# Optimization experiments

Hardware: AMD Instinct MI355X
Metric: run time of the kernel (lower is better)

Reference implementation:

```python
import jax, jax.numpy as jnp
from jax import lax
import numpy as np


def setup_inputs() -> dict:
    key = jax.random.key(0)
    k1, k2 = jax.random.split(key)
    x = jax.random.normal(k1, (16, 512, 512, 3), dtype=jnp.float32)
    # raw filter; module draws N(mean=10, scale=1) then normalizes to sum 1
    filt = jax.random.normal(k2, (9, 9, 1, 1), dtype=jnp.float32)
    return {"x": x, "filt": filt}


def _conv_same(a, f):
    # NHWC input, HWIO filter, SAME padding, stride 1
    return lax.conv_general_dilated(
        a, f, window_strides=(1, 1), padding="SAME",
        dimension_numbers=("NHWC", "HWIO", "NHWC"))


def reference(x, filt):
    # Keras: random_normal_variable(mean=10, scale=1) -> shift raw N(0,1) by 10
    f = filt + 10.0
    f = f / jnp.sum(f)                      # normalize BEFORE channel repeat
    f = jnp.tile(f, (1, 1, 3, 1))           # (9,9,3,1): sums over 3 input channels
    local_mean = _conv_same(x, f)           # (B,H,W,1), broadcasts over channels
    v = x - local_mean                      # (B,H,W,3)
    sigma = jnp.sqrt(_conv_same(v * v, f))  # (B,H,W,1)
    mean = jnp.mean(sigma, axis=(1, 2), keepdims=True)  # (B,1,1,1)
    return v / jnp.maximum(mean, sigma)
```

## Files before the change

### kernel.cpp

```cpp
#include <hip/hip_runtime.h>

#define BATCH 16
#define HH 512
#define WW 512
#define NPIX (BATCH * HH * WW)

#define TW 32
#define TH 8
#define ROWS 4
#define OTH (TH*ROWS)
#define RAD 4
#define LW (TW + 2 * RAD)
#define LH (OTH + 2 * RAD)

__global__ void norm_filter_kernel(const float* __restrict__ filt,
                                   float* __restrict__ f) {
    __shared__ float sh[128];
    int tid = threadIdx.x;
    float v = (tid < 81) ? (filt[tid] + 10.0f) : 0.0f;
    sh[tid] = v;
    __syncthreads();
    for (int o = 64; o > 0; o >>= 1) {
        if (tid < o) sh[tid] += sh[tid + o];
        __syncthreads();
    }
    float sum = sh[0];
    if (tid < 81) f[tid] = v / sum;
}

__global__ __launch_bounds__(256) void conv_mean_kernel(
        const float* __restrict__ x, const float* __restrict__ f,
        float* __restrict__ m, float* __restrict__ t) {
    __shared__ float tile[LH][LW];
    __shared__ float fs[81];

    const int tx = threadIdx.x, ty = threadIdx.y;
    const int tid = ty * TW + tx;
    const int b = blockIdx.z;
    const int h0 = blockIdx.y * OTH;
    const int w0 = blockIdx.x * TW;
    const float* xb = x + (size_t)b * HH * WW * 3;

    for (int i = tid; i < LH * LW; i += 256) {
        int r = i / LW, c = i - r * LW;
        int gh = h0 - RAD + r, gw = w0 - RAD + c;
        float v = 0.0f;
        if (gh >= 0 && gh < HH && gw >= 0 && gw < WW) {
            const float* xp = xb + ((size_t)gh * WW + gw) * 3;
            v = xp[0] + xp[1] + xp[2];
        }
        tile[r][c] = v;
    }
    if (tid < 81) fs[tid] = f[tid];
    __syncthreads();

    const int r0 = ty * ROWS;
    float acc[ROWS] = {0.f, 0.f, 0.f, 0.f};
#pragma unroll
    for (int tr = 0; tr < ROWS + 8; tr++) {
        float v[9];
#pragma unroll
        for (int j = 0; j < 9; j++) v[j] = tile[r0 + tr][tx + j];
#pragma unroll
        for (int o = 0; o < ROWS; o++) {
            const int dh = tr - o;
            if (dh >= 0 && dh < 9) {
#pragma unroll
                for (int j = 0; j < 9; j++) acc[o] += v[j] * fs[dh * 9 + j];
            }
        }
    }

#pragma unroll
    for (int o = 0; o < ROWS; o++) {
        const int h = h0 + r0 + o, w = w0 + tx;
        const size_t idx = ((size_t)b * HH + h) * WW + w;
        m[idx] = acc[o];
        const float* xp = xb + ((size_t)h * WW + w) * 3;
        float d0 = xp[0] - acc[o];
        float d1 = xp[1] - acc[o];
        float d2 = xp[2] - acc[o];
        t[idx] = d0 * d0 + d1 * d1 + d2 * d2;
    }
}

__global__ __launch_bounds__(256) void conv_sigma_kernel(
        const float* __restrict__ t, const float* __restrict__ f,
        float* __restrict__ sig, float* __restrict__ partial) {
    __shared__ float tile[LH][LW];
    __shared__ float fs[81];
    __shared__ float wsum[4];

    const int tx = threadIdx.x, ty = threadIdx.y;
    const int tid = ty * TW + tx;
    const int b = blockIdx.z;
    const int h0 = blockIdx.y * OTH;
    const int w0 = blockIdx.x * TW;
    const float* tb = t + (size_t)b * HH * WW;

    for (int i = tid; i < LH * LW; i += 256) {
        int r = i / LW, c = i - r * LW;
        int gh = h0 - RAD + r, gw = w0 - RAD + c;
        float v = 0.0f;
        if (gh >= 0 && gh < HH && gw >= 0 && gw < WW) {
            v = tb[(size_t)gh * WW + gw];
        }
        tile[r][c] = v;
    }
    if (tid < 81) fs[tid] = f[tid];
    __syncthreads();

    const int r0 = ty * ROWS;
    float acc[ROWS] = {0.f, 0.f, 0.f, 0.f};
#pragma unroll
    for (int tr = 0; tr < ROWS + 8; tr++) {
        float v[9];
#pragma unroll
        for (int j = 0; j < 9; j++) v[j] = tile[r0 + tr][tx + j];
#pragma unroll
        for (int o = 0; o < ROWS; o++) {
            const int dh = tr - o;
            if (dh >= 0 && dh < 9) {
#pragma unroll
                for (int j = 0; j < 9; j++) acc[o] += v[j] * fs[dh * 9 + j];
            }
        }
    }

    float psum = 0.0f;
#pragma unroll
    for (int o = 0; o < ROWS; o++) {
        float sg = sqrtf(fmaxf(acc[o], 0.0f));
        const int h = h0 + r0 + o, w = w0 + tx;
        sig[((size_t)b * HH + h) * WW + w] = sg;
        psum += sg;
    }

#pragma unroll
    for (int o = 32; o > 0; o >>= 1) psum += __shfl_down(psum, o);
    if ((tid & 63) == 0) wsum[tid >> 6] = psum;
    __syncthreads();
    if (tid == 0)
        partial[b * 256 + blockIdx.y * 16 + blockIdx.x] =
            wsum[0] + wsum[1] + wsum[2] + wsum[3];
}

__global__ __launch_bounds__(256) void reduce_bsum_kernel(
        const float* __restrict__ partial, float* __restrict__ bsum) {
    __shared__ float wsum[4];
    const int b = blockIdx.x, tid = threadIdx.x;
    float v = partial[b * 256 + tid];
#pragma unroll
    for (int o = 32; o > 0; o >>= 1) v += __shfl_down(v, o);
    if ((tid & 63) == 0) wsum[tid >> 6] = v;
    __syncthreads();
    if (tid == 0) bsum[b] = wsum[0] + wsum[1] + wsum[2] + wsum[3];
}

__global__ __launch_bounds__(256) void final_kernel(
        const float* __restrict__ x, const float* __restrict__ m,
        const float* __restrict__ sig, const float* __restrict__ bsum,
        float* __restrict__ out) {
    const int i = blockIdx.x * 256 + threadIdx.x;
    const int b = i >> 16;
    const float mean = bsum[b] * (1.0f / (HH * WW));

    float4 mv = ((const float4*)m)[i];
    float4 sv = ((const float4*)sig)[i];
    const float4* xp = (const float4*)x + (size_t)i * 3;
    float4 a = xp[0], bb = xp[1], cc = xp[2];

    float d0 = fmaxf(mean, sv.x);
    float d1 = fmaxf(mean, sv.y);
    float d2 = fmaxf(mean, sv.z);
    float d3 = fmaxf(mean, sv.w);

    float4 o0, o1, o2;
    o0.x = (a.x - mv.x) / d0;
    o0.y = (a.y - mv.x) / d0;
    o0.z = (a.z - mv.x) / d0;
    o0.w = (a.w - mv.y) / d1;
    o1.x = (bb.x - mv.y) / d1;
    o1.y = (bb.y - mv.y) / d1;
    o1.z = (bb.z - mv.z) / d2;
    o1.w = (bb.w - mv.z) / d2;
    o2.x = (cc.x - mv.z) / d2;
    o2.y = (cc.y - mv.w) / d3;
    o2.z = (cc.z - mv.w) / d3;
    o2.w = (cc.w - mv.w) / d3;

    float4* op = (float4*)out + (size_t)i * 3;
    op[0] = o0;
    op[1] = o1;
    op[2] = o2;
}

extern "C" void kernel_launch(void* const* d_in, const int* in_sizes, int n_in,
                              void* d_out, int out_size, void* d_ws, size_t ws_size,
                              hipStream_t stream) {
    const float* x = (const float*)d_in[0];
    const float* filt = (const float*)d_in[1];
    float* out = (float*)d_out;

    char* ws = (char*)d_ws;
    float* f = (float*)ws;
    float* bsum = (float*)(ws + 512);
    float* partial = (float*)(ws + 1024);
    float* m = (float*)(ws + 32768);
    float* t = m + NPIX;
    float* sig = t + NPIX;

    norm_filter_kernel<<<1, 128, 0, stream>>>(filt, f);

    dim3 cblock(TW, TH);
    dim3 cgrid(WW / TW, HH / OTH, BATCH);
    conv_mean_kernel<<<cgrid, cblock, 0, stream>>>(x, f, m, t);
    conv_sigma_kernel<<<cgrid, cblock, 0, stream>>>(t, f, sig, partial);
    reduce_bsum_kernel<<<BATCH, 256, 0, stream>>>(partial, bsum);

    final_kernel<<<NPIX / 4 / 256, 256, 0, stream>>>(x, m, sig, bsum, out);
}
```

Baseline: 154.9 us.

## Fuse filter normalization, mean conv and sigma conv into one tiled kernel

Merges the filter-normalization kernel and both 9x9 convolutions into a single kernel per 32x32 output tile. The mean is computed on a halo-extended 40x40 region in shared memory, and the squared deviation is rebuilt algebraically from per-pixel channel sums and sums of squares, so no intermediate t buffer goes through global memory. This removes two launches and a full write and read of t. The cost is redundant halo computation for the first convolution, larger shared-memory use that may lower occupancy, and idle threads in the first stage, since only 240 of 256 threads take part.

Result: slower. 177.4 us (+14.5%).

```diff
diff --git a/kernel.cpp b/kernel.cpp
--- a/kernel.cpp
+++ b/kernel.cpp
@@ -5,135 +5,122 @@
 #define WW 512
 #define NPIX (BATCH * HH * WW)
 
-#define TW 32
-#define TH 8
-#define ROWS 4
-#define OTH (TH*ROWS)
 #define RAD 4
-#define LW (TW + 2 * RAD)
-#define LH (OTH + 2 * RAD)
-
-__global__ void norm_filter_kernel(const float* __restrict__ filt,
-                                   float* __restrict__ f) {
-    __shared__ float sh[128];
-    int tid = threadIdx.x;
-    float v = (tid < 81) ? (filt[tid] + 10.0f) : 0.0f;
-    sh[tid] = v;
-    __syncthreads();
-    for (int o = 64; o > 0; o >>= 1) {
-        if (tid < o) sh[tid] += sh[tid + o];
-        __syncthreads();
-    }
-    float sum = sh[0];
-    if (tid < 81) f[tid] = v / sum;
-}
-
-__global__ __launch_bounds__(256) void conv_mean_kernel(
-        const float* __restrict__ x, const float* __restrict__ f,
-        float* __restrict__ m, float* __restrict__ t) {
-    __shared__ float tile[LH][LW];
+#define OT 32
+#define MT (OT + 2*RAD)
+#define ST (MT + 2*RAD)
+
+__global__ __launch_bounds__(256) void lcn_fused_kernel(
+        const float* __restrict__ x, const float* __restrict__ filt,
+        float* __restrict__ m, float* __restrict__ sig,
+        float* __restrict__ partial) {
+    __shared__ float s48[ST][ST];
+    __shared__ float q48[ST][ST];
+    __shared__ float t40[MT][MT];
     __shared__ float fs[81];
-
-    const int tx = threadIdx.x, ty = threadIdx.y;
-    const int tid = ty * TW + tx;
+    __shared__ float fsum_sh;
+    __shared__ float wsum[4];
+
+    const int tid = threadIdx.x;
     const int b = blockIdx.z;
-    const int h0 = blockIdx.y * OTH;
-    const int w0 = blockIdx.x * TW;
+    const int h0 = blockIdx.y * OT;
+    const int w0 = blockIdx.x * OT;
     const float* xb = x + (size_t)b * HH * WW * 3;
 
-    for (int i = tid; i < LH * LW; i += 256) {
-        int r = i / LW, c = i - r * LW;
-        int gh = h0 - RAD + r, gw = w0 - RAD + c;
-        float v = 0.0f;
+    if (tid < 64) {
+        float v = filt[tid] + 10.0f;
+        if (tid < 17) v += filt[tid + 64] + 10.0f;
+#pragma unroll
+        for (int o = 32; o > 0; o >>= 1) v += __shfl_down(v, o);
+        if (tid == 0) fsum_sh = v;
+    }
+
+    for (int i = tid; i < ST * ST; i += 256) {
+        int r = i / ST, c = i - r * ST;
+        int gh = h0 - 2 * RAD + r, gw = w0 - 2 * RAD + c;
+        float sv = 0.0f, qv = 0.0f;
         if (gh >= 0 && gh < HH && gw >= 0 && gw < WW) {
             const float* xp = xb + ((size_t)gh * WW + gw) * 3;
-            v = xp[0] + xp[1] + xp[2];
-        }
-        tile[r][c] = v;
-    }
-    if (tid < 81) fs[tid] = f[tid];
-    __syncthreads();
-
-    const int r0 = ty * ROWS;
-    float acc[ROWS] = {0.f, 0.f, 0.f, 0.f};
-#pragma unroll
-    for (int tr = 0; tr < ROWS + 8; tr++) {
-        float v[9];
-#pragma unroll
-        for (int j = 0; j < 9; j++) v[j] = tile[r0 + tr][tx + j];
-#pragma unroll
-        for (int o = 0; o < ROWS; o++) {
-            const int dh = tr - o;
-            if (dh >= 0 && dh < 9) {
-#pragma unroll
-                for (int j = 0; j < 9; j++) acc[o] += v[j] * fs[dh * 9 + j];
+            float a0 = xp[0], a1 = xp[1], a2 = xp[2];
+            sv = a0 + a1 + a2;
+            qv = a0 * a0 + a1 * a1 + a2 * a2;
+        }
+        s48[r][c] = sv;
+        q48[r][c] = qv;
+    }
+    __syncthreads();
+
+    if (tid < 81) fs[tid] = (filt[tid] + 10.0f) / fsum_sh;
+    __syncthreads();
+
+    {
+        const int c2 = tid % MT;
+        const int g = tid / MT;
+        if (g < 6) {
+            const int rbeg = g * 7;
+            const int rcnt = (rbeg + 7 <= MT) ? 7 : (MT - rbeg);
+            float acc[7] = {0.f, 0.f, 0.f, 0.f, 0.f, 0.f, 0.f};
+            for (int tr = 0; tr < rcnt + 8; tr++) {
+                float v[9];
+#pragma unroll
+                for (int j = 0; j < 9; j++) v[j] = s48[rbeg + tr][c2 + j];
+#pragma unroll
+                for (int o = 0; o < 7; o++) {
+                    const int dh = tr - o;
+                    if (o < rcnt && dh >= 0 && dh < 9) {
+                        float a = 0.0f;
+#pragma unroll
+                        for (int j = 0; j < 9; j++) a += v[j] * fs[dh * 9 + j];
+                        acc[o] += a;
+                    }
+                }
             }
-        }
-    }
-
-#pragma unroll
-    for (int o = 0; o < ROWS; o++) {
-        const int h = h0 + r0 + o, w = w0 + tx;
-        const size_t idx = ((size_t)b * HH + h) * WW + w;
-        m[idx] = acc[o];
-        const float* xp = xb + ((size_t)h * WW + w) * 3;
-        float d0 = xp[0] - acc[o];
-        float d1 = xp[1] - acc[o];
-        float d2 = xp[2] - acc[o];
-        t[idx] = d0 * d0 + d1 * d1 + d2 * d2;
-    }
-}
-
-__global__ __launch_bounds__(256) void conv_sigma_kernel(
-        const float* __restrict__ t, const float* __restrict__ f,
-        float* __restrict__ sig, float* __restrict__ partial) {
-    __shared__ float tile[LH][LW];
-    __shared__ float fs[81];
-    __shared__ float wsum[4];
-
-    const int tx = threadIdx.x, ty = threadIdx.y;
-    const int tid = ty * TW + tx;
-    const int b = blockIdx.z;
-    const int h0 = blockIdx.y * OTH;
-    const int w0 = blockIdx.x * TW;
-    const float* tb = t + (size_t)b * HH * WW;
-
-    for (int i = tid; i < LH * LW; i += 256) {
-        int r = i / LW, c = i - r * LW;
-        int gh = h0 - RAD + r, gw = w0 - RAD + c;
-        float v = 0.0f;
-        if (gh >= 0 && gh < HH && gw >= 0 && gw < WW) {
-            v = tb[(size_t)gh * WW + gw];
-        }
-        tile[r][c] = v;
-    }
-    if (tid < 81) fs[tid] = f[tid];
-    __syncthreads();
-
-    const int r0 = ty * ROWS;
-    float acc[ROWS] = {0.f, 0.f, 0.f, 0.f};
-#pragma unroll
-    for (int tr = 0; tr < ROWS + 8; tr++) {
-        float v[9];
-#pragma unroll
-        for (int j = 0; j < 9; j++) v[j] = tile[r0 + tr][tx + j];
-#pragma unroll
-        for (int o = 0; o < ROWS; o++) {
-            const int dh = tr - o;
-            if (dh >= 0 && dh < 9) {
-#pragma unroll
-                for (int j = 0; j < 9; j++) acc[o] += v[j] * fs[dh * 9 + j];
+            for (int o = 0; o < rcnt; o++) {
+                const int rr = rbeg + o;
+                const int gh = h0 - RAD + rr, gw = w0 - RAD + c2;
+                const float mv = acc[o];
+                const float sc = s48[rr + RAD][c2 + RAD];
+                const float qc = q48[rr + RAD][c2 + RAD];
+                const bool inimg = (gh >= 0 && gh < HH && gw >= 0 && gw < WW);
+                t40[rr][c2] = inimg ? (qc - 2.0f * mv * sc + 3.0f * mv * mv)
+                                    : 0.0f;
+                if (rr >= RAD && rr < RAD + OT && c2 >= RAD && c2 < RAD + OT) {
+                    m[((size_t)b * HH + gh) * WW + gw] = mv;
+                }
             }
         }
     }
+    __syncthreads();
 
     float psum = 0.0f;
-#pragma unroll
-    for (int o = 0; o < ROWS; o++) {
-        float sg = sqrtf(fmaxf(acc[o], 0.0f));
-        const int h = h0 + r0 + o, w = w0 + tx;
-        sig[((size_t)b * HH + h) * WW + w] = sg;
-        psum += sg;
+    {
+        const int c3 = tid % OT;
+        const int g3 = tid / OT;
+        const int rbeg = g3 * 4;
+        float acc[4] = {0.f, 0.f, 0.f, 0.f};
+#pragma unroll
+        for (int tr = 0; tr < 12; tr++) {
+            float v[9];
+#pragma unroll
+            for (int j = 0; j < 9; j++) v[j] = t40[rbeg + tr][c3 + j];
+#pragma unroll
+            for (int o = 0; o < 4; o++) {
+                const int dh = tr - o;
+                if (dh >= 0 && dh < 9) {
+                    float a = 0.0f;
+#pragma unroll
+                    for (int j = 0; j < 9; j++) a += v[j] * fs[dh * 9 + j];
+                    acc[o] += a;
+                }
+            }
+        }
+#pragma unroll
+        for (int o = 0; o < 4; o++) {
+            const float sg = sqrtf(fmaxf(acc[o], 0.0f));
+            const int h = h0 + rbeg + o, w = w0 + c3;
+            sig[((size_t)b * HH + h) * WW + w] = sg;
+            psum += sg;
+        }
     }
 
 #pragma unroll
@@ -203,20 +190,13 @@
     float* out = (float*)d_out;
 
     char* ws = (char*)d_ws;
-    float* f = (float*)ws;
     float* bsum = (float*)(ws + 512);
     float* partial = (float*)(ws + 1024);
     float* m = (float*)(ws + 32768);
-    float* t = m + NPIX;
-    float* sig = t + NPIX;
-
-    norm_filter_kernel<<<1, 128, 0, stream>>>(filt, f);
-
-    dim3 cblock(TW, TH);
-    dim3 cgrid(WW / TW, HH / OTH, BATCH);
-    conv_mean_kernel<<<cgrid, cblock, 0, stream>>>(x, f, m, t);
-    conv_sigma_kernel<<<cgrid, cblock, 0, stream>>>(t, f, sig, partial);
+    float* sig = m + NPIX;
+
+    dim3 cgrid(WW / OT, HH / OT, BATCH);
+    lcn_fused_kernel<<<cgrid, 256, 0, stream>>>(x, filt, m, sig, partial);
     reduce_bsum_kernel<<<BATCH, 256, 0, stream>>>(partial, bsum);
-
     final_kernel<<<NPIX / 4 / 256, 256, 0, stream>>>(x, m, sig, bsum, out);
 }
```
